# Optimization experiments

Hardware: AMD Instinct MI355X
Metric: run time of the kernel (lower is better)

## Reference

```python
import jax, jax.numpy as jnp
import numpy as np


def setup_inputs() -> dict:
    key = jax.random.key(0)
    k1, k2, k3 = jax.random.split(key, 3)
    N, C_in, H, W = 32, 16, 256, 256
    C_out, K = 64, 3
    x = jax.random.normal(k1, (N, C_in, H, W), dtype=jnp.float32)
    # match nn.Conv2d default init scale roughly (values irrelevant for correctness harness)
    fan_in = C_in * K * K
    bound = 1.0 / np.sqrt(fan_in)
    conv_weight = jax.random.normal(k2, (C_out, C_in, K, K), dtype=jnp.float32) * bound
    conv_bias = jax.random.normal(k3, (C_out,), dtype=jnp.float32) * bound
    return {"x": x, "conv_weight": conv_weight, "conv_bias": conv_bias}


def reference(x, conv_weight, conv_bias):
    # Conv2d: stride=1, padding=0 (VALID), dilation=1, groups=1
    y = jax.lax.conv_general_dilated(
        x, conv_weight,
        window_strides=(1, 1), padding='VALID',
        dimension_numbers=('NCHW', 'OIHW', 'NCHW'),
    ) + conv_bias[None, :, None, None]          # (N, C_out, OH, OW)
    y = jnp.min(y, axis=1, keepdims=True)       # min over output channels -> (N, 1, OH, OW)
    return jnp.tanh(jnp.tanh(y))                # double tanh
```

## Files before the change

kernel.cpp:

```cpp
#include <hip/hip_runtime.h>
#include <hip/hip_bf16.h>

typedef __attribute__((ext_vector_type(8))) short short8;
typedef __attribute__((ext_vector_type(4))) float f32x4;

#define CIN   16
#define COUT  64
#define HH    256
#define WW    256
#define OHH   254
#define OWW   254

#define HSTR   (36 * 8)
#define HALFU  (34 * HSTR)

__device__ __forceinline__ ushort f2bf(float f) {
    unsigned u = __builtin_bit_cast(unsigned, f);
    unsigned r = (u + 0x7fffu + ((u >> 16) & 1u)) >> 16;
    return (ushort)r;
}

__device__ __forceinline__ float dtanh2(float x) {
    const float K = 2.8853900817779268f;
    float xc = fminf(fmaxf(x, -9.0f), 9.0f);
    float e1 = __builtin_amdgcn_exp2f(K * xc);
    float t1 = 1.0f - 2.0f * __builtin_amdgcn_rcpf(e1 + 1.0f);
    float e2 = __builtin_amdgcn_exp2f(K * t1);
    return 1.0f - 2.0f * __builtin_amdgcn_rcpf(e2 + 1.0f);
}

__global__ void prep_weights(const float* __restrict__ wsrc, ushort* __restrict__ wfrag) {
    int idx = blockIdx.x * 256 + threadIdx.x;
    if (idx >= 10240) return;
    int r    = idx & 7;
    int lane = (idx >> 3) & 63;
    int j    = (idx >> 9) & 3;
    int p    = idx >> 11;
    int kl   = ((lane >> 4) << 3) + r;
    int tap  = 2 * p + (kl >> 4);
    int ci   = kl & 15;
    int co   = j * 16 + (lane & 15);
    float v = 0.0f;
    if (tap <= 8) {
        int kh = tap / 3, kw = tap - 3 * (tap / 3);
        v = wsrc[(co * CIN + ci) * 9 + kh * 3 + kw];
    }
    wfrag[idx] = f2bf(v);
}

__global__ __launch_bounds__(256, 3) void conv_min_tanh(
        const float* __restrict__ x, const ushort* __restrict__ wfrag,
        const float* __restrict__ bias, float* __restrict__ out) {
    __shared__ ushort lds[2 * HALFU];

    const int tid = threadIdx.x;
    const int n   = blockIdx.z;
    const int oh0 = blockIdx.y * 32;
    const int ow0 = blockIdx.x * 32;
    const int HW  = HH * WW;

    const float* xb = x + (size_t)n * CIN * HW;
    auto stage_pos = [&](int pos) {
        int hp  = pos / 36;
        int r2  = pos - hp * 36;
        int ciq = r2 / 9;
        int w4  = r2 - ciq * 9;
        int hg  = min(oh0 + hp, HH - 1);
        int wg  = min(ow0 + 4 * w4, WW - 4);
        const float* src = xb + (size_t)(ciq * 4) * HW + hg * WW + wg;
        f32x4 v0 = *reinterpret_cast<const f32x4*>(src);
        f32x4 v1 = *reinterpret_cast<const f32x4*>(src + HW);
        f32x4 v2 = *reinterpret_cast<const f32x4*>(src + 2 * HW);
        f32x4 v3 = *reinterpret_cast<const f32x4*>(src + 3 * HW);
        ushort* dst = &lds[(ciq >> 1) * HALFU + (hp * 36 + 4 * w4) * 8 + (ciq & 1) * 4];
#pragma unroll
        for (int e = 0; e < 4; ++e) {
            unsigned lo, hi;
            asm("v_cvt_pk_bf16_f32 %0, %1, %2" : "=v"(lo) : "v"(v0[e]), "v"(v1[e]));
            asm("v_cvt_pk_bf16_f32 %0, %1, %2" : "=v"(hi) : "v"(v2[e]), "v"(v3[e]));
            uint2 pk; pk.x = lo; pk.y = hi;
            *reinterpret_cast<uint2*>(dst + e * 8) = pk;
        }
    };
#pragma unroll
    for (int it = 0; it < 4; ++it) stage_pos(tid + it * 256);
    if (tid < 1224 - 1024) stage_pos(tid + 1024);

    const int lane = tid & 63;
    const int wid  = tid >> 6;
    const int g    = lane >> 4;
    const int mm   = lane & 15;

    short8 wf0[5], wf1[5], wf2[5], wf3[5];
#pragma unroll
    for (int p = 0; p < 5; ++p) {
        wf0[p] = *reinterpret_cast<const short8*>(wfrag + (((p * 4 + 0) * 64 + lane) * 8));
        wf1[p] = *reinterpret_cast<const short8*>(wfrag + (((p * 4 + 1) * 64 + lane) * 8));
        wf2[p] = *reinterpret_cast<const short8*>(wfrag + (((p * 4 + 2) * 64 + lane) * 8));
        wf3[p] = *reinterpret_cast<const short8*>(wfrag + (((p * 4 + 3) * 64 + lane) * 8));
    }
    const f32x4 bi0 = *reinterpret_cast<const f32x4*>(bias +  0 + 4 * g);
    const f32x4 bi1 = *reinterpret_cast<const f32x4*>(bias + 16 + 4 * g);
    const f32x4 bi2 = *reinterpret_cast<const f32x4*>(bias + 32 + 4 * g);
    const f32x4 bi3 = *reinterpret_cast<const f32x4*>(bias + 48 + 4 * g);

    __syncthreads();

#pragma unroll
    for (int ch = 0; ch < 2; ++ch) {
        const ushort* bp[5];
#pragma unroll
        for (int p = 0; p < 5; ++p) {
            int tap = 2 * p + (g >> 1);
            if (tap > 8) tap = 8;
            int kh = tap / 3, kw = tap - 3 * (tap / 3);
            bp[p] = &lds[(g & 1) * HALFU + (wid * 8 + kh) * HSTR + (ch * 16 + mm + kw) * 8];
        }
#pragma unroll
        for (int i = 0; i < 8; ++i) {
            f32x4 a0 = bi0, a1 = bi1, a2 = bi2, a3 = bi3;
#pragma unroll
            for (int p = 0; p < 5; ++p) {
                short8 b = *reinterpret_cast<const short8*>(bp[p] + i * HSTR);
                a0 = __builtin_amdgcn_mfma_f32_16x16x32_bf16(wf0[p], b, a0, 0, 0, 0);
                a1 = __builtin_amdgcn_mfma_f32_16x16x32_bf16(wf1[p], b, a1, 0, 0, 0);
                a2 = __builtin_amdgcn_mfma_f32_16x16x32_bf16(wf2[p], b, a2, 0, 0, 0);
                a3 = __builtin_amdgcn_mfma_f32_16x16x32_bf16(wf3[p], b, a3, 0, 0, 0);
            }
            float v = fminf(fminf(fminf(a0[0], a0[1]), fminf(a0[2], a0[3])),
                            fminf(fminf(a1[0], a1[1]), fminf(a1[2], a1[3])));
            v = fminf(v, fminf(fminf(fminf(a2[0], a2[1]), fminf(a2[2], a2[3])),
                               fminf(fminf(a3[0], a3[1]), fminf(a3[2], a3[3]))));
            v = fminf(v, __shfl_xor(v, 16, 64));
            v = fminf(v, __shfl_xor(v, 32, 64));
            const float y = dtanh2(v);
            const int oh = oh0 + wid * 8 + i;
            const int ow = ow0 + ch * 16 + mm;
            if (lane < 16 && oh < OHH && ow < OWW)
                out[((size_t)n * OHH + oh) * OWW + ow] = y;
        }
    }
}

extern "C" void kernel_launch(void* const* d_in, const int* in_sizes, int n_in,
                              void* d_out, int out_size, void* d_ws, size_t ws_size,
                              hipStream_t stream) {
    const float* x = (const float*)d_in[0];
    const float* w = (const float*)d_in[1];
    const float* b = (const float*)d_in[2];
    float* out     = (float*)d_out;
    ushort* wfrag  = (ushort*)d_ws;

    prep_weights<<<40, 256, 0, stream>>>(w, wfrag);
    dim3 grid(8, 8, 32);
    conv_min_tanh<<<grid, dim3(256, 1, 1), 0, stream>>>(x, wfrag, b, out);
}
```

Before: 61.78 us.

## Process four images per block with double-buffered LDS prefetch of next image

Each block now loops over four batch images, loading the next image's input tile into registers while computing on the current LDS buffer, then writing it to a second LDS buffer. The goal is to hide global load latency behind MFMA work and to amortise the weight-fragment loads across images. In exchange LDS use doubles, staging needs many more registers, occupancy is lowered to 2 blocks per CU, and the grid shrinks to 512 blocks.

```diff
diff --git a/kernel.cpp b/kernel.cpp
--- a/kernel.cpp
+++ b/kernel.cpp
@@ -13,6 +13,7 @@
 
 #define HSTR   (36 * 8)
 #define HALFU  (34 * HSTR)
+#define BUFU   (2 * HALFU)
 
 __device__ __forceinline__ ushort f2bf(float f) {
     unsigned u = __builtin_bit_cast(unsigned, f);
@@ -48,43 +49,57 @@
     wfrag[idx] = f2bf(v);
 }
 
-__global__ __launch_bounds__(256, 3) void conv_min_tanh(
+__global__ __launch_bounds__(256, 2) void conv_min_tanh(
         const float* __restrict__ x, const ushort* __restrict__ wfrag,
         const float* __restrict__ bias, float* __restrict__ out) {
-    __shared__ ushort lds[2 * HALFU];
+    __shared__ ushort lds[2 * BUFU];
 
     const int tid = threadIdx.x;
-    const int n   = blockIdx.z;
     const int oh0 = blockIdx.y * 32;
     const int ow0 = blockIdx.x * 32;
+    const int n0  = blockIdx.z * 4;
     const int HW  = HH * WW;
 
-    const float* xb = x + (size_t)n * CIN * HW;
-    auto stage_pos = [&](int pos) {
+    int goff[5], loff[5];
+#pragma unroll
+    for (int s = 0; s < 5; ++s) {
+        int pos = tid + s * 256;
+        if (pos > 1223) pos = 1223;
         int hp  = pos / 36;
         int r2  = pos - hp * 36;
         int ciq = r2 / 9;
         int w4  = r2 - ciq * 9;
         int hg  = min(oh0 + hp, HH - 1);
         int wg  = min(ow0 + 4 * w4, WW - 4);
-        const float* src = xb + (size_t)(ciq * 4) * HW + hg * WW + wg;
-        f32x4 v0 = *reinterpret_cast<const f32x4*>(src);
-        f32x4 v1 = *reinterpret_cast<const f32x4*>(src + HW);
-        f32x4 v2 = *reinterpret_cast<const f32x4*>(src + 2 * HW);
-        f32x4 v3 = *reinterpret_cast<const f32x4*>(src + 3 * HW);
-        ushort* dst = &lds[(ciq >> 1) * HALFU + (hp * 36 + 4 * w4) * 8 + (ciq & 1) * 4];
+        goff[s] = (ciq * 4) * HW + hg * WW + wg;
+        loff[s] = (ciq >> 1) * HALFU + (hp * 36 + 4 * w4) * 8 + (ciq & 1) * 4;
+    }
+
+    f32x4 r[5][4];
+    auto load_all = [&](const float* xb) {
 #pragma unroll
-        for (int e = 0; e < 4; ++e) {
-            unsigned lo, hi;
-            asm("v_cvt_pk_bf16_f32 %0, %1, %2" : "=v"(lo) : "v"(v0[e]), "v"(v1[e]));
-            asm("v_cvt_pk_bf16_f32 %0, %1, %2" : "=v"(hi) : "v"(v2[e]), "v"(v3[e]));
-            uint2 pk; pk.x = lo; pk.y = hi;
-            *reinterpret_cast<uint2*>(dst + e * 8) = pk;
+        for (int s = 0; s < 5; ++s) {
+            const float* src = xb + goff[s];
+            r[s][0] = *reinterpret_cast<const f32x4*>(src);
+            r[s][1] = *reinterpret_cast<const f32x4*>(src + HW);
+            r[s][2] = *reinterpret_cast<const f32x4*>(src + 2 * HW);
+            r[s][3] = *reinterpret_cast<const f32x4*>(src + 3 * HW);
         }
     };
+    auto write_all = [&](int base) {
 #pragma unroll
-    for (int it = 0; it < 4; ++it) stage_pos(tid + it * 256);
-    if (tid < 1224 - 1024) stage_pos(tid + 1024);
+        for (int s = 0; s < 5; ++s) {
+            ushort* dst = &lds[base + loff[s]];
+#pragma unroll
+            for (int e = 0; e < 4; ++e) {
+                unsigned lo, hi;
+                asm("v_cvt_pk_bf16_f32 %0, %1, %2" : "=v"(lo) : "v"(r[s][0][e]), "v"(r[s][1][e]));
+                asm("v_cvt_pk_bf16_f32 %0, %1, %2" : "=v"(hi) : "v"(r[s][2][e]), "v"(r[s][3][e]));
+                uint2 pk; pk.x = lo; pk.y = hi;
+                *reinterpret_cast<uint2*>(dst + e * 8) = pk;
+            }
+        }
+    };
 
     const int lane = tid & 63;
     const int wid  = tid >> 6;
@@ -104,41 +119,59 @@
     const f32x4 bi2 = *reinterpret_cast<const f32x4*>(bias + 32 + 4 * g);
     const f32x4 bi3 = *reinterpret_cast<const f32x4*>(bias + 48 + 4 * g);
 
+    int boff[5];
+#pragma unroll
+    for (int p = 0; p < 5; ++p) {
+        int tap = 2 * p + (g >> 1);
+        if (tap > 8) tap = 8;
+        int kh = tap / 3, kw = tap - 3 * (tap / 3);
+        boff[p] = (g & 1) * HALFU + (wid * 8 + kh) * HSTR + (mm + kw) * 8;
+    }
+
+    auto compute = [&](int base, int n) {
+#pragma unroll
+        for (int ch = 0; ch < 2; ++ch) {
+#pragma unroll
+            for (int i = 0; i < 8; ++i) {
+                f32x4 a0 = bi0, a1 = bi1, a2 = bi2, a3 = bi3;
+#pragma unroll
+                for (int p = 0; p < 5; ++p) {
+                    short8 b = *reinterpret_cast<const short8*>(
+                        &lds[base + boff[p] + ch * 128 + i * HSTR]);
+                    a0 = __builtin_amdgcn_mfma_f32_16x16x32_bf16(wf0[p], b, a0, 0, 0, 0);
+                    a1 = __builtin_amdgcn_mfma_f32_16x16x32_bf16(wf1[p], b, a1, 0, 0, 0);
+                    a2 = __builtin_amdgcn_mfma_f32_16x16x32_bf16(wf2[p], b, a2, 0, 0, 0);
+                    a3 = __builtin_amdgcn_mfma_f32_16x16x32_bf16(wf3[p], b, a3, 0, 0, 0);
+                }
+                float v = fminf(fminf(fminf(a0[0], a0[1]), fminf(a0[2], a0[3])),
+                                fminf(fminf(a1[0], a1[1]), fminf(a1[2], a1[3])));
+                v = fminf(v, fminf(fminf(fminf(a2[0], a2[1]), fminf(a2[2], a2[3])),
+                                   fminf(fminf(a3[0], a3[1]), fminf(a3[2], a3[3]))));
+                v = fminf(v, __shfl_xor(v, 16, 64));
+                v = fminf(v, __shfl_xor(v, 32, 64));
+                const float y = dtanh2(v);
+                const int oh = oh0 + wid * 8 + i;
+                const int ow = ow0 + ch * 16 + mm;
+                if (lane < 16 && oh < OHH && ow < OWW)
+                    out[((size_t)n * OHH + oh) * OWW + ow] = y;
+            }
+        }
+    };
+
+    load_all(x + (size_t)n0 * CIN * HW);
+    write_all(0);
     __syncthreads();
-
-#pragma unroll
-    for (int ch = 0; ch < 2; ++ch) {
-        const ushort* bp[5];
-#pragma unroll
-        for (int p = 0; p < 5; ++p) {
-            int tap = 2 * p + (g >> 1);
-            if (tap > 8) tap = 8;
-            int kh = tap / 3, kw = tap - 3 * (tap / 3);
-            bp[p] = &lds[(g & 1) * HALFU + (wid * 8 + kh) * HSTR + (ch * 16 + mm + kw) * 8];
-        }
-#pragma unroll
-        for (int i = 0; i < 8; ++i) {
-            f32x4 a0 = bi0, a1 = bi1, a2 = bi2, a3 = bi3;
-#pragma unroll
-            for (int p = 0; p < 5; ++p) {
-                short8 b = *reinterpret_cast<const short8*>(bp[p] + i * HSTR);
-                a0 = __builtin_amdgcn_mfma_f32_16x16x32_bf16(wf0[p], b, a0, 0, 0, 0);
-                a1 = __builtin_amdgcn_mfma_f32_16x16x32_bf16(wf1[p], b, a1, 0, 0, 0);
-                a2 = __builtin_amdgcn_mfma_f32_16x16x32_bf16(wf2[p], b, a2, 0, 0, 0);
-                a3 = __builtin_amdgcn_mfma_f32_16x16x32_bf16(wf3[p], b, a3, 0, 0, 0);
-            }
-            float v = fminf(fminf(fminf(a0[0], a0[1]), fminf(a0[2], a0[3])),
-                            fminf(fminf(a1[0], a1[1]), fminf(a1[2], a1[3])));
-            v = fminf(v, fminf(fminf(fminf(a2[0], a2[1]), fminf(a2[2], a2[3])),
-                               fminf(fminf(a3[0], a3[1]), fminf(a3[2], a3[3]))));
-            v = fminf(v, __shfl_xor(v, 16, 64));
-            v = fminf(v, __shfl_xor(v, 32, 64));
-            const float y = dtanh2(v);
-            const int oh = oh0 + wid * 8 + i;
-            const int ow = ow0 + ch * 16 + mm;
-            if (lane < 16 && oh < OHH && ow < OWW)
-                out[((size_t)n * OHH + oh) * OWW + ow] = y;
-        }
+    int cur = 0;
+    for (int t = 0; t < 4; ++t) {
+        if (t < 3)
+            load_all(x + (size_t)(n0 + t + 1) * CIN * HW);
+        __builtin_amdgcn_sched_barrier(0);
+        compute(cur * BUFU, n0 + t);
+        __builtin_amdgcn_sched_barrier(0);
+        if (t < 3)
+            write_all((cur ^ 1) * BUFU);
+        cur ^= 1;
+        __syncthreads();
     }
 }
 
@@ -152,6 +185,6 @@
     ushort* wfrag  = (ushort*)d_ws;
 
     prep_weights<<<40, 256, 0, stream>>>(w, wfrag);
-    dim3 grid(8, 8, 32);
+    dim3 grid(8, 8, 8);
     conv_min_tanh<<<grid, dim3(256, 1, 1), 0, stream>>>(x, wfrag, b, out);
 }
```

Measured after the change: 72.13 us. 1.17x slower.

## Switch conv MFMA from 16x16x32 to 32x32x16 with per-tap K split

Applied to the files above, without the earlier changes.

Replaces the 16x16x32 bf16 MFMA tiling, which packed pairs of taps into K=32 and padded the tenth tap slot with zeros, with 32x32x16 MFMAs that take one tap (16 input channels) per instruction and cover 32 pixels by 32 output channels. This removes the wasted zero-padded tap work and the separate two-chunk loop over output columns, and cuts the cross-lane min to a single shuffle. The weight prep kernel is rewritten for the new fragment layout and the LDS halves get an 8-element pad. In exchange each wave holds 32 accumulator registers and 18 weight fragments, which raises register pressure and may affect occupancy under the 3-blocks launch bound.

```diff
diff --git a/kernel.cpp b/kernel.cpp
--- a/kernel.cpp
+++ b/kernel.cpp
@@ -1,8 +1,9 @@
 #include <hip/hip_runtime.h>
 #include <hip/hip_bf16.h>
 
-typedef __attribute__((ext_vector_type(8))) short short8;
-typedef __attribute__((ext_vector_type(4))) float f32x4;
+typedef __attribute__((ext_vector_type(8)))  short short8;
+typedef __attribute__((ext_vector_type(4)))  float f32x4;
+typedef __attribute__((ext_vector_type(16))) float f32x16;
 
 #define CIN   16
 #define COUT  64
@@ -12,7 +13,7 @@
 #define OWW   254
 
 #define HSTR   (36 * 8)
-#define HALFU  (34 * HSTR)
+#define HALF   (34 * HSTR + 8)
 
 __device__ __forceinline__ ushort f2bf(float f) {
     unsigned u = __builtin_bit_cast(unsigned, f);
@@ -31,27 +32,21 @@
 
 __global__ void prep_weights(const float* __restrict__ wsrc, ushort* __restrict__ wfrag) {
     int idx = blockIdx.x * 256 + threadIdx.x;
-    if (idx >= 10240) return;
+    if (idx >= 9216) return;
     int r    = idx & 7;
     int lane = (idx >> 3) & 63;
-    int j    = (idx >> 9) & 3;
-    int p    = idx >> 11;
-    int kl   = ((lane >> 4) << 3) + r;
-    int tap  = 2 * p + (kl >> 4);
-    int ci   = kl & 15;
-    int co   = j * 16 + (lane & 15);
-    float v = 0.0f;
-    if (tap <= 8) {
-        int kh = tap / 3, kw = tap - 3 * (tap / 3);
-        v = wsrc[(co * CIN + ci) * 9 + kh * 3 + kw];
-    }
-    wfrag[idx] = f2bf(v);
+    int j    = (idx >> 9) & 1;
+    int tap  = idx >> 10;
+    int ci   = 8 * (lane >> 5) + r;
+    int co   = j * 32 + (lane & 31);
+    int kh   = tap / 3, kw = tap - 3 * kh;
+    wfrag[idx] = f2bf(wsrc[(co * CIN + ci) * 9 + kh * 3 + kw]);
 }
 
 __global__ __launch_bounds__(256, 3) void conv_min_tanh(
         const float* __restrict__ x, const ushort* __restrict__ wfrag,
         const float* __restrict__ bias, float* __restrict__ out) {
-    __shared__ ushort lds[2 * HALFU];
+    __shared__ ushort lds[2 * HALF];
 
     const int tid = threadIdx.x;
     const int n   = blockIdx.z;
@@ -72,7 +67,7 @@
         f32x4 v1 = *reinterpret_cast<const f32x4*>(src + HW);
         f32x4 v2 = *reinterpret_cast<const f32x4*>(src + 2 * HW);
         f32x4 v3 = *reinterpret_cast<const f32x4*>(src + 3 * HW);
-        ushort* dst = &lds[(ciq >> 1) * HALFU + (hp * 36 + 4 * w4) * 8 + (ciq & 1) * 4];
+        ushort* dst = &lds[(ciq >> 1) * HALF + (hp * 36 + 4 * w4) * 8 + (ciq & 1) * 4];
 #pragma unroll
         for (int e = 0; e < 4; ++e) {
             unsigned lo, hi;
@@ -86,59 +81,53 @@
     for (int it = 0; it < 4; ++it) stage_pos(tid + it * 256);
     if (tid < 1224 - 1024) stage_pos(tid + 1024);
 
-    const int lane = tid & 63;
-    const int wid  = tid >> 6;
-    const int g    = lane >> 4;
-    const int mm   = lane & 15;
+    const int lane  = tid & 63;
+    const int wid   = tid >> 6;
+    const int px    = lane & 31;
+    const int khalf = lane >> 5;
 
-    short8 wf0[5], wf1[5], wf2[5], wf3[5];
+    short8 wf[9][2];
 #pragma unroll
-    for (int p = 0; p < 5; ++p) {
-        wf0[p] = *reinterpret_cast<const short8*>(wfrag + (((p * 4 + 0) * 64 + lane) * 8));
-        wf1[p] = *reinterpret_cast<const short8*>(wfrag + (((p * 4 + 1) * 64 + lane) * 8));
-        wf2[p] = *reinterpret_cast<const short8*>(wfrag + (((p * 4 + 2) * 64 + lane) * 8));
-        wf3[p] = *reinterpret_cast<const short8*>(wfrag + (((p * 4 + 3) * 64 + lane) * 8));
+    for (int tap = 0; tap < 9; ++tap) {
+        wf[tap][0] = *reinterpret_cast<const short8*>(wfrag + ((tap * 2 + 0) * 64 + lane) * 8);
+        wf[tap][1] = *reinterpret_cast<const short8*>(wfrag + ((tap * 2 + 1) * 64 + lane) * 8);
     }
-    const f32x4 bi0 = *reinterpret_cast<const f32x4*>(bias +  0 + 4 * g);
-    const f32x4 bi1 = *reinterpret_cast<const f32x4*>(bias + 16 + 4 * g);
-    const f32x4 bi2 = *reinterpret_cast<const f32x4*>(bias + 32 + 4 * g);
-    const f32x4 bi3 = *reinterpret_cast<const f32x4*>(bias + 48 + 4 * g);
+    f32x16 bi0, bi1;
+#pragma unroll
+    for (int q = 0; q < 4; ++q) {
+        f32x4 b0 = *reinterpret_cast<const f32x4*>(bias +  0 + 4 * khalf + 8 * q);
+        f32x4 b1 = *reinterpret_cast<const f32x4*>(bias + 32 + 4 * khalf + 8 * q);
+#pragma unroll
+        for (int s = 0; s < 4; ++s) { bi0[q * 4 + s] = b0[s]; bi1[q * 4 + s] = b1[s]; }
+    }
+
+    const ushort* bp[9];
+#pragma unroll
+    for (int tap = 0; tap < 9; ++tap) {
+        int kh = tap / 3, kw = tap - 3 * kh;
+        bp[tap] = &lds[khalf * HALF + (wid * 8 + kh) * HSTR + (px + kw) * 8];
+    }
 
     __syncthreads();
 
 #pragma unroll
-    for (int ch = 0; ch < 2; ++ch) {
-        const ushort* bp[5];
+    for (int i = 0; i < 8; ++i) {
+        f32x16 a0 = bi0, a1 = bi1;
 #pragma unroll
-        for (int p = 0; p < 5; ++p) {
-            int tap = 2 * p + (g >> 1);
-            if (tap > 8) tap = 8;
-            int kh = tap / 3, kw = tap - 3 * (tap / 3);
-            bp[p] = &lds[(g & 1) * HALFU + (wid * 8 + kh) * HSTR + (ch * 16 + mm + kw) * 8];
+        for (int tap = 0; tap < 9; ++tap) {
+            short8 b = *reinterpret_cast<const short8*>(bp[tap] + i * HSTR);
+            a0 = __builtin_amdgcn_mfma_f32_32x32x16_bf16(wf[tap][0], b, a0, 0, 0, 0);
+            a1 = __builtin_amdgcn_mfma_f32_32x32x16_bf16(wf[tap][1], b, a1, 0, 0, 0);
         }
+        float v = fminf(a0[0], a1[0]);
 #pragma unroll
-        for (int i = 0; i < 8; ++i) {
-            f32x4 a0 = bi0, a1 = bi1, a2 = bi2, a3 = bi3;
-#pragma unroll
-            for (int p = 0; p < 5; ++p) {
-                short8 b = *reinterpret_cast<const short8*>(bp[p] + i * HSTR);
-                a0 = __builtin_amdgcn_mfma_f32_16x16x32_bf16(wf0[p], b, a0, 0, 0, 0);
-                a1 = __builtin_amdgcn_mfma_f32_16x16x32_bf16(wf1[p], b, a1, 0, 0, 0);
-                a2 = __builtin_amdgcn_mfma_f32_16x16x32_bf16(wf2[p], b, a2, 0, 0, 0);
-                a3 = __builtin_amdgcn_mfma_f32_16x16x32_bf16(wf3[p], b, a3, 0, 0, 0);
-            }
-            float v = fminf(fminf(fminf(a0[0], a0[1]), fminf(a0[2], a0[3])),
-                            fminf(fminf(a1[0], a1[1]), fminf(a1[2], a1[3])));
-            v = fminf(v, fminf(fminf(fminf(a2[0], a2[1]), fminf(a2[2], a2[3])),
-                               fminf(fminf(a3[0], a3[1]), fminf(a3[2], a3[3]))));
-            v = fminf(v, __shfl_xor(v, 16, 64));
-            v = fminf(v, __shfl_xor(v, 32, 64));
-            const float y = dtanh2(v);
-            const int oh = oh0 + wid * 8 + i;
-            const int ow = ow0 + ch * 16 + mm;
-            if (lane < 16 && oh < OHH && ow < OWW)
-                out[((size_t)n * OHH + oh) * OWW + ow] = y;
-        }
+        for (int r = 1; r < 16; ++r) v = fminf(v, fminf(a0[r], a1[r]));
+        v = fminf(v, __shfl_xor(v, 32, 64));
+        const float y  = dtanh2(v);
+        const int   oh = oh0 + wid * 8 + i;
+        const int   ow = ow0 + px;
+        if (lane < 32 && oh < OHH && ow < OWW)
+            out[((size_t)n * OHH + oh) * OWW + ow] = y;
     }
 }
 
@@ -151,7 +140,7 @@
     float* out     = (float*)d_out;
     ushort* wfrag  = (ushort*)d_ws;
 
-    prep_weights<<<40, 256, 0, stream>>>(w, wfrag);
+    prep_weights<<<36, 256, 0, stream>>>(w, wfrag);
     dim3 grid(8, 8, 32);
     conv_min_tanh<<<grid, dim3(256, 1, 1), 0, stream>>>(x, wfrag, b, out);
 }
```

Result: slower. 63.30 us (+2.4%).
